# Performance work log

Measured on AMD Instinct MI355X. Metric: run time of the kernel, lower is better.

## Reference

```python
import jax, jax.numpy as jnp
import numpy as np

T, B, IN, H = 2048, 2048, 5, 10


def setup_inputs() -> dict:
    key = jax.random.key(0)
    ks = jax.random.split(key, 7)
    return {
        "x": jax.random.normal(ks[0], (T, B, IN), dtype=jnp.float32),
        "hx0": jax.random.uniform(ks[1], (B, H), dtype=jnp.float32),
        "cx0": jax.random.uniform(ks[2], (B, H), dtype=jnp.float32),
        "W_ih": jax.random.normal(ks[3], (4 * H, IN), dtype=jnp.float32) * 0.3,
        "W_hh": jax.random.normal(ks[4], (4 * H, H), dtype=jnp.float32) * 0.3,
        "b_ih": jax.random.normal(ks[5], (4 * H,), dtype=jnp.float32) * 0.1,
        "b_hh": jax.random.normal(ks[6], (4 * H,), dtype=jnp.float32) * 0.1,
    }


def reference(x, hx0, cx0, W_ih, W_hh, b_ih, b_hh):
    # torch.nn.LSTMCell gate order: i, f, g, o
    bias = b_ih + b_hh  # [4H]

    def step(carry, xt):
        h, c = carry  # [B, H] each
        gates = xt @ W_ih.T + h @ W_hh.T + bias  # [B, 4H]
        i, f, g, o = jnp.split(gates, 4, axis=-1)
        c_new = jax.nn.sigmoid(f) * c + jax.nn.sigmoid(i) * jnp.tanh(g)
        h_new = jax.nn.sigmoid(o) * jnp.tanh(c_new)
        return (h_new, c_new), h_new

    _, hs = jax.lax.scan(step, (hx0, cx0), x)  # hs: [T, B, H]
    # original concatenates per-step hx along dim 0 -> [T*B, H]
    return hs.reshape(-1, hs.shape[-1])
```

## Files before the change

### kernel.cpp

```cpp
#include <hip/hip_runtime.h>


#define T_STEPS 2048
#define BATCH   2048
#define NIN     5
#define NH      10
#define PF      8

typedef float v2f __attribute__((ext_vector_type(2)));

__device__ __forceinline__ float hw_exp2(float v) { return __builtin_amdgcn_exp2f(v); }
__device__ __forceinline__ float hw_rcp(float v)  { return __builtin_amdgcn_rcpf(v); }
__device__ __forceinline__ float readlane_f(float v, int srclane) {
    return __builtin_bit_cast(float,
        __builtin_amdgcn_readlane(__builtin_bit_cast(int, v), srclane));
}
__device__ __forceinline__ v2f splat2(float v) { v2f r; r.x = v; r.y = v; return r; }

__global__ __launch_bounds__(64, 2) void lstm_fused_kernel(
    const float* __restrict__ x,   const float* __restrict__ hx0,
    const float* __restrict__ cx0, const float* __restrict__ Wih,
    const float* __restrict__ Whh, const float* __restrict__ bih,
    const float* __restrict__ bhh, float* __restrict__ out)
{
    const float L2E2  = 2.8853900817779268f;
    const float NL2E  = -1.4426950408889634f;
    const float NL2E2 = -2.8853900817779268f;

    const int lane = threadIdx.x;
    int j = lane;
    if (j > NH - 1) j = NH - 1;
    const bool jval = (lane < NH);

    const int b = blockIdx.x;

    const int ri = j, rf = NH + j, rg = 2 * NH + j, ro = 3 * NH + j;

    v2f wxif[NIN], wxgo[NIN], whif[NH], whgo[NH];
#pragma unroll
    for (int k = 0; k < NIN; ++k) {
        wxif[k].x = NL2E  * Wih[ri * NIN + k];  wxif[k].y = NL2E * Wih[rf * NIN + k];
        wxgo[k].x = NL2E2 * Wih[rg * NIN + k];  wxgo[k].y = NL2E * Wih[ro * NIN + k];
    }
#pragma unroll
    for (int k = 0; k < NH; ++k) {
        whif[k].x = NL2E  * Whh[ri * NH + k];   whif[k].y = NL2E * Whh[rf * NH + k];
        whgo[k].x = NL2E2 * Whh[rg * NH + k];   whgo[k].y = NL2E * Whh[ro * NH + k];
    }
    v2f bif, bgo;
    bif.x = NL2E  * (bih[ri] + bhh[ri]);  bif.y = NL2E * (bih[rf] + bhh[rf]);
    bgo.x = NL2E2 * (bih[rg] + bhh[rg]);  bgo.y = NL2E * (bih[ro] + bhh[ro]);

    float hv[NH];
#pragma unroll
    for (int k = 0; k < NH; ++k) hv[k] = hx0[b * NH + k];
    float cs2 = NL2E2 * cx0[b * NH + j];

    int vzero;
    asm volatile("v_mov_b32 %0, 0" : "=v"(vzero));
    const float* xb = x + (size_t)b * NIN + vzero;

    float xr[PF][NIN];
#pragma unroll
    for (int q = 0; q < PF; ++q)
#pragma unroll
        for (int k = 0; k < NIN; ++k)
            xr[q][k] = xb[(size_t)q * (BATCH * NIN) + k];

    float* outp = out + (size_t)b * NH + j;

#define LSTM_STEP(QQ, TT, DO_REFILL)                                          \
    {                                                                         \
                   \
        v2f aif0 = bif, ago0 = bgo;                                           \
        v2f aif1 = splat2(0.0f), ago1 = splat2(0.0f);                         \
        {                                                                     \
            v2f xx0 = splat2(xr[QQ][0]);                                      \
            v2f xx1 = splat2(xr[QQ][1]);                                      \
            v2f xx2 = splat2(xr[QQ][2]);                                      \
            v2f xx3 = splat2(xr[QQ][3]);                                      \
            v2f xx4 = splat2(xr[QQ][4]);                                      \
            aif0 += xx0 * wxif[0];  ago0 += xx0 * wxgo[0];                    \
            aif1 += xx1 * wxif[1];  ago1 += xx1 * wxgo[1];                    \
            aif0 += xx2 * wxif[2];  ago0 += xx2 * wxgo[2];                    \
            aif1 += xx3 * wxif[3];  ago1 += xx3 * wxgo[3];                    \
            aif0 += xx4 * wxif[4];  ago0 += xx4 * wxgo[4];                    \
        }                                                                     \
        if (DO_REFILL) {                                                      \
            const int tn = (TT) + PF;                                         \
            _Pragma("unroll")                                                 \
            for (int k = 0; k < NIN; ++k)                                     \
                xr[QQ][k] = xb[(size_t)tn * (BATCH * NIN) + k];               \
        }                                                                     \
            \
        _Pragma("unroll")                                                     \
        for (int k = 0; k < NH; k += 2) {                                     \
            v2f h0 = splat2(hv[k]);                                           \
            v2f h1 = splat2(hv[k + 1]);                                       \
            aif0 += h0 * whif[k];      ago0 += h0 * whgo[k];                  \
            aif1 += h1 * whif[k + 1];  ago1 += h1 * whgo[k + 1];              \
        }                                                                     \
        const v2f aif = aif0 + aif1;                                          \
        const v2f ago = ago0 + ago1;                                          \
                          \
        const float si  = hw_rcp(1.0f + hw_exp2(aif.x));                      \
        const float sf  = hw_rcp(1.0f + hw_exp2(aif.y));                      \
        const float rg_ = hw_rcp(1.0f + hw_exp2(ago.x));                      \
        const float so  = hw_rcp(1.0f + hw_exp2(ago.y));                      \
        const float tg2 = fmaf(-2.0f * L2E2, rg_, L2E2);   \
        cs2 = fmaf(sf, cs2, si * tg2);            \
        const float tc = fmaf(2.0f, hw_rcp(1.0f + hw_exp2(cs2)), -1.0f);      \
        const float h  = so * tc;                                             \
        if (jval) outp[(size_t)(TT) * (BATCH * NH)] = h;                      \
             \
        _Pragma("unroll")                                                     \
        for (int k = 0; k < NH; ++k)                                          \
            hv[k] = readlane_f(h, k);                                         \
    }

#pragma unroll 1
    for (int t0 = 0; t0 < T_STEPS - PF; t0 += PF) {
#pragma unroll
        for (int q = 0; q < PF; ++q) {
            LSTM_STEP(q, t0 + q, 1);
        }
    }
    {
        const int t0 = T_STEPS - PF;
#pragma unroll
        for (int q = 0; q < PF; ++q) {
            LSTM_STEP(q, t0 + q, 0);
        }
    }
#undef LSTM_STEP
}

extern "C" void kernel_launch(void* const* d_in, const int* in_sizes, int n_in,
                              void* d_out, int out_size, void* d_ws, size_t ws_size,
                              hipStream_t stream) {
    const float* x   = (const float*)d_in[0];
    const float* hx0 = (const float*)d_in[1];
    const float* cx0 = (const float*)d_in[2];
    const float* Wih = (const float*)d_in[3];
    const float* Whh = (const float*)d_in[4];
    const float* bih = (const float*)d_in[5];
    const float* bhh = (const float*)d_in[6];
    float* out = (float*)d_out;

    lstm_fused_kernel<<<BATCH, 64, 0, stream>>>(x, hx0, cx0, Wih, Whh, bih, bhh, out);
}
```

Baseline: 862.1 us.

## Pack two batch elements per wavefront using both 32-lane halves

After: 858.4 us. No clear change (-0.4%).

```diff
diff --git a/kernel.cpp b/kernel.cpp
--- a/kernel.cpp
+++ b/kernel.cpp
@@ -5,7 +5,7 @@
 #define BATCH   2048
 #define NIN     5
 #define NH      10
-#define PF      8
+#define PF      4
 
 typedef float v2f __attribute__((ext_vector_type(2)));
 
@@ -17,7 +17,7 @@
 }
 __device__ __forceinline__ v2f splat2(float v) { v2f r; r.x = v; r.y = v; return r; }
 
-__global__ __launch_bounds__(64, 2) void lstm_fused_kernel(
+__global__ __launch_bounds__(64, 1) void lstm_fused_kernel(
     const float* __restrict__ x,   const float* __restrict__ hx0,
     const float* __restrict__ cx0, const float* __restrict__ Wih,
     const float* __restrict__ Whh, const float* __restrict__ bih,
@@ -28,11 +28,12 @@
     const float NL2E2 = -2.8853900817779268f;
 
     const int lane = threadIdx.x;
-    int j = lane;
+    const int half = lane >> 5;
+    int j = lane & 31;
     if (j > NH - 1) j = NH - 1;
-    const bool jval = (lane < NH);
+    const bool lo = (lane < 32);
 
-    const int b = blockIdx.x;
+    const int b = blockIdx.x * 2 + half;
 
     const int ri = j, rf = NH + j, rg = 2 * NH + j, ro = 3 * NH + j;
 
@@ -56,22 +57,19 @@
     for (int k = 0; k < NH; ++k) hv[k] = hx0[b * NH + k];
     float cs2 = NL2E2 * cx0[b * NH + j];
 
-    int vzero;
-    asm volatile("v_mov_b32 %0, 0" : "=v"(vzero));
-    const float* xb = x + (size_t)b * NIN + vzero;
-
+    const float* xb = x + (size_t)b * NIN;
     float xr[PF][NIN];
 #pragma unroll
     for (int q = 0; q < PF; ++q)
 #pragma unroll
         for (int k = 0; k < NIN; ++k)
-            xr[q][k] = xb[(size_t)q * (BATCH * NIN) + k];
+            xr[q][k] = xb[q * (BATCH * NIN) + k];
 
     float* outp = out + (size_t)b * NH + j;
 
 #define LSTM_STEP(QQ, TT, DO_REFILL)                                          \
     {                                                                         \
-                   \
+                                                \
         v2f aif0 = bif, ago0 = bgo;                                           \
         v2f aif1 = splat2(0.0f), ago1 = splat2(0.0f);                         \
         {                                                                     \
@@ -87,12 +85,12 @@
             aif0 += xx4 * wxif[4];  ago0 += xx4 * wxgo[4];                    \
         }                                                                     \
         if (DO_REFILL) {                                                      \
-            const int tn = (TT) + PF;                                         \
+            const int tn = (TT) + PF;       \
             _Pragma("unroll")                                                 \
             for (int k = 0; k < NIN; ++k)                                     \
-                xr[QQ][k] = xb[(size_t)tn * (BATCH * NIN) + k];               \
+                xr[QQ][k] = xb[tn * (BATCH * NIN) + k];                       \
         }                                                                     \
-            \
+             \
         _Pragma("unroll")                                                     \
         for (int k = 0; k < NH; k += 2) {                                     \
             v2f h0 = splat2(hv[k]);                                           \
@@ -111,26 +109,30 @@
         cs2 = fmaf(sf, cs2, si * tg2);            \
         const float tc = fmaf(2.0f, hw_rcp(1.0f + hw_exp2(cs2)), -1.0f);      \
         const float h  = so * tc;                                             \
-        if (jval) outp[(size_t)(TT) * (BATCH * NH)] = h;                      \
              \
+        outp[(TT) * (BATCH * NH)] = h;                                        \
+                 \
         _Pragma("unroll")                                                     \
-        for (int k = 0; k < NH; ++k)                                          \
-            hv[k] = readlane_f(h, k);                                         \
+        for (int k = 0; k < NH; ++k) {                                        \
+            const float hA = readlane_f(h, k);                                \
+            const float hB = readlane_f(h, 32 + k);                           \
+            hv[k] = lo ? hA : hB;                                             \
+        }                                                                     \
     }
 
 #pragma unroll 1
     for (int t0 = 0; t0 < T_STEPS - PF; t0 += PF) {
-#pragma unroll
-        for (int q = 0; q < PF; ++q) {
-            LSTM_STEP(q, t0 + q, 1);
-        }
+        LSTM_STEP(0, t0 + 0, 1)
+        LSTM_STEP(1, t0 + 1, 1)
+        LSTM_STEP(2, t0 + 2, 1)
+        LSTM_STEP(3, t0 + 3, 1)
     }
     {
         const int t0 = T_STEPS - PF;
-#pragma unroll
-        for (int q = 0; q < PF; ++q) {
-            LSTM_STEP(q, t0 + q, 0);
-        }
+        LSTM_STEP(0, t0 + 0, 0)
+        LSTM_STEP(1, t0 + 1, 0)
+        LSTM_STEP(2, t0 + 2, 0)
+        LSTM_STEP(3, t0 + 3, 0)
     }
 #undef LSTM_STEP
 }
@@ -147,5 +149,5 @@
     const float* bhh = (const float*)d_in[6];
     float* out = (float*)d_out;
 
-    lstm_fused_kernel<<<BATCH, 64, 0, stream>>>(x, hx0, cx0, Wih, Whh, bih, bhh, out);
+    lstm_fused_kernel<<<BATCH / 2, 64, 0, stream>>>(x, hx0, cx0, Wih, Whh, bih, bhh, out);
 }
```
